# Kernel optimization log

Measured on AMD Instinct MI355X. Metric: run time of the kernel, lower is better.

## Reference

```python
import jax, jax.numpy as jnp
import numpy as np

B, Q, H, HKV, D = 4, 1024, 32, 8, 128
HID = H * D            # 4096
BS = 16                # block_size
BLOCKS_PER_SEQ = Q // BS  # 64
NB = B * BLOCKS_PER_SEQ   # 256 total cache blocks
THETA = 10000.0
SCALE = D ** -0.5


def _rope(x, pos):
    # x: [T, h, D] (NeoX half-split rotary), pos: [T] int
    inv = 1.0 / (THETA ** (jnp.arange(0, D, 2, dtype=jnp.float32) / D))  # [D/2]
    ang = pos[:, None].astype(jnp.float32) * inv                          # [T, D/2]
    cos = jnp.cos(ang)[:, None, :]
    sin = jnp.sin(ang)[:, None, :]
    x1, x2 = jnp.split(x, 2, axis=-1)
    return jnp.concatenate([x1 * cos - x2 * sin, x1 * sin + x2 * cos], axis=-1).astype(x.dtype)


def setup_inputs() -> dict:
    key = jax.random.key(0)
    ks = jax.random.split(key, 3)
    hidden_states = jax.random.normal(ks[0], (B * Q, HID), dtype=jnp.float32)
    w_qkv = jax.random.normal(ks[1], (HID, (H + 2 * HKV) * D), dtype=jnp.float32) * 0.02
    w_o = jax.random.normal(ks[2], (H * D, HID), dtype=jnp.float32) * 0.02
    key_cache = jnp.zeros((NB, BS, HKV, D), dtype=jnp.float32)
    value_cache = jnp.zeros((NB, BS, HKV, D), dtype=jnp.float32)
    positions = jnp.tile(jnp.arange(Q, dtype=jnp.int32), B)          # context_len=0 prefill
    slot_mapping = jnp.arange(B * Q, dtype=jnp.int32)                # contiguous slots
    block_tables = jnp.arange(NB, dtype=jnp.int32).reshape(B, BLOCKS_PER_SEQ)
    return {"hidden_states": hidden_states, "w_qkv": w_qkv, "w_o": w_o,
            "key_cache": key_cache, "value_cache": value_cache,
            "positions": positions, "slot_mapping": slot_mapping,
            "block_tables": block_tables}


def reference(hidden_states, w_qkv, w_o, key_cache, value_cache, positions, slot_mapping, block_tables):
    # QKV projection and split (q_size = H*D, kv_size = HKV*D)
    qkv = hidden_states @ w_qkv
    q, k, v = jnp.split(qkv, [H * D, H * D + HKV * D], axis=-1)
    q = q.reshape(-1, H, D)
    k = k.reshape(-1, HKV, D)
    v = v.reshape(-1, HKV, D)
    q = _rope(q, positions)
    k = _rope(k, positions)
    # BlockedKVCache.write: slot -> (slot // BS, slot % BS); flatten block dims
    kc = key_cache.reshape(NB * BS, HKV, D).at[slot_mapping].set(k)
    vc = value_cache.reshape(NB * BS, HKV, D).at[slot_mapping].set(v)
    # BlockedKVCache.gather via block_table: [B, blocks, BS, HKV, D] -> [B, S, HKV, D]
    gk = kc.reshape(NB, BS, HKV, D)[block_tables].reshape(B, Q, HKV, D)
    gv = vc.reshape(NB, BS, HKV, D)[block_tables].reshape(B, Q, HKV, D)
    # repeat_kv (GQA): each kv head repeated consecutively
    rep = H // HKV
    gk = jnp.repeat(gk, rep, axis=2)   # [B, S, H, D]
    gv = jnp.repeat(gv, rep, axis=2)
    qb = q.reshape(B, Q, H, D)
    scores = jnp.einsum('bqhd,bshd->bhqs', qb, gk) * SCALE
    # visible = context_len + token_idx + 1 with context_len=0 -> causal mask
    causal = jnp.arange(Q)[None, :] <= jnp.arange(Q)[:, None]          # [q, s]
    scores = jnp.where(causal[None, None], scores.astype(jnp.float32), -jnp.inf)
    probs = jax.nn.softmax(scores, axis=-1).astype(qb.dtype)
    attn = jnp.einsum('bhqs,bshd->bqhd', probs, gv).reshape(B * Q, H * D)
    return attn @ w_o
```

## Files before the change

### kernel.cpp

```cpp
#include <hip/hip_runtime.h>
#include <stdint.h>

typedef short short8  __attribute__((ext_vector_type(8)));
typedef short short4v __attribute__((ext_vector_type(4)));
typedef float f32x4   __attribute__((ext_vector_type(4)));

#define B_    4
#define Q_    1024
#define H_    32
#define HKV_  8
#define D_    128
#define HID_  4096
#define NQKV_ 6144
#define SCALE_ 0.08838834764831845f

__device__ __forceinline__ short f2bf(float f) {
  unsigned u = __builtin_bit_cast(unsigned, f);
  u += 0x7fffu + ((u >> 16) & 1u);
  return (short)(u >> 16);
}
__device__ __forceinline__ float bf2f(short s) {
  unsigned u = ((unsigned)(unsigned short)s) << 16;
  return __builtin_bit_cast(float, u);
}

__device__ __forceinline__ void gload_lds16(const void* g, void* l) {
  __builtin_amdgcn_global_load_lds(
      (__attribute__((address_space(1))) void*)(uintptr_t)(g),
      (__attribute__((address_space(3))) void*)(l), 16, 0, 0);
}

__device__ __forceinline__ f32x4 mfma16x16x32(short8 a, short8 b, f32x4 c) {
  return __builtin_amdgcn_mfma_f32_16x16x32_bf16(a, b, c, 0, 0, 0);
}

__global__ __launch_bounds__(256) void k_cvt(const float* __restrict__ src,
                                             short* __restrict__ dst, int n) {
  int i = (blockIdx.x * 256 + threadIdx.x) * 4;
  if (i + 3 < n) {
    float4 v = *reinterpret_cast<const float4*>(src + i);
    short4v o;
    o[0] = f2bf(v.x); o[1] = f2bf(v.y); o[2] = f2bf(v.z); o[3] = f2bf(v.w);
    *reinterpret_cast<short4v*>(dst + i) = o;
  }
}

__global__ __launch_bounds__(256) void k_cvt_t(const float* __restrict__ src,
                                               short* __restrict__ dst, int R, int C) {
  __shared__ float tile[32][33];
  int c0 = blockIdx.x * 32, r0 = blockIdx.y * 32;
  int tx = threadIdx.x & 31, ty = threadIdx.x >> 5;
#pragma unroll
  for (int i = 0; i < 4; ++i)
    tile[ty + i * 8][tx] = src[(size_t)(r0 + ty + i * 8) * C + c0 + tx];
  __syncthreads();
#pragma unroll
  for (int i = 0; i < 4; ++i)
    dst[(size_t)(c0 + ty + i * 8) * R + r0 + tx] = f2bf(tile[tx][ty + i * 8]);
}

__global__ __launch_bounds__(256) void k_gemm1(const short* __restrict__ A,
                                               const short* __restrict__ Bt,
                                               short* __restrict__ qout,
                                               short* __restrict__ kvout) {
  __shared__ alignas(16) short Asm[128 * 32];
  __shared__ alignas(16) short Bsm[128 * 32];
  const int tid = threadIdx.x;
  const int wave = tid >> 6, lane = tid & 63;
  const int G = lane >> 4, r = lane & 15;
  const int wm = wave >> 1, wn = wave & 1;
  const size_t Arow0 = (size_t)blockIdx.y * 128;
  const size_t Brow0 = (size_t)blockIdx.x * 128;
  const int K = HID_;
  const int ldrow = lane >> 2, ldcol = (lane & 3) * 8;
  short* Cb; size_t ldc, cb;
  if (Brow0 < (size_t)HID_) { Cb = qout; ldc = HID_; cb = Brow0; }
  else                      { Cb = kvout; ldc = 2048; cb = Brow0 - HID_; }
  f32x4 acc[4][4] = {};
  for (int k0 = 0; k0 < K; k0 += 32) {
    __syncthreads();
#pragma unroll
    for (int i = 0; i < 2; ++i) {
      int c = wave * 2 + i;
      gload_lds16(A + (Arow0 + c * 16 + ldrow) * K + k0 + ldcol, &Asm[c * 512]);
      gload_lds16(Bt + (Brow0 + c * 16 + ldrow) * K + k0 + ldcol, &Bsm[c * 512]);
    }
    asm volatile("s_waitcnt vmcnt(0)" ::: "memory");
    __syncthreads();
    short8 af[4], bf[4];
#pragma unroll
    for (int i = 0; i < 4; ++i)
      af[i] = *reinterpret_cast<const short8*>(&Asm[(wm * 64 + i * 16 + r) * 32 + G * 8]);
#pragma unroll
    for (int j = 0; j < 4; ++j)
      bf[j] = *reinterpret_cast<const short8*>(&Bsm[(wn * 64 + j * 16 + r) * 32 + G * 8]);
#pragma unroll
    for (int i = 0; i < 4; ++i)
#pragma unroll
      for (int j = 0; j < 4; ++j)
        acc[i][j] = mfma16x16x32(af[i], bf[j], acc[i][j]);
  }
#pragma unroll
  for (int i = 0; i < 4; ++i)
#pragma unroll
    for (int j = 0; j < 4; ++j)
#pragma unroll
      for (int rr = 0; rr < 4; ++rr) {
        size_t row = Arow0 + wm * 64 + i * 16 + G * 4 + rr;
        size_t col = cb + wn * 64 + j * 16 + r;
        Cb[row * ldc + col] = f2bf(acc[i][j][rr]);
      }
}

__global__ __launch_bounds__(256) void k_gemm2(const short* __restrict__ A,
                                               const short* __restrict__ Bt,
                                               float* __restrict__ C) {
  __shared__ alignas(16) short Asm[128 * 32];
  __shared__ alignas(16) short Bsm[128 * 32];
  const int tid = threadIdx.x;
  const int wave = tid >> 6, lane = tid & 63;
  const int G = lane >> 4, r = lane & 15;
  const int wm = wave >> 1, wn = wave & 1;
  const size_t Arow0 = (size_t)blockIdx.y * 128;
  const size_t Brow0 = (size_t)blockIdx.x * 128;
  const int K = HID_;
  const int ldrow = lane >> 2, ldcol = (lane & 3) * 8;
  f32x4 acc[4][4] = {};
  for (int k0 = 0; k0 < K; k0 += 32) {
    __syncthreads();
#pragma unroll
    for (int i = 0; i < 2; ++i) {
      int c = wave * 2 + i;
      gload_lds16(A + (Arow0 + c * 16 + ldrow) * K + k0 + ldcol, &Asm[c * 512]);
      gload_lds16(Bt + (Brow0 + c * 16 + ldrow) * K + k0 + ldcol, &Bsm[c * 512]);
    }
    asm volatile("s_waitcnt vmcnt(0)" ::: "memory");
    __syncthreads();
    short8 af[4], bf[4];
#pragma unroll
    for (int i = 0; i < 4; ++i)
      af[i] = *reinterpret_cast<const short8*>(&Asm[(wm * 64 + i * 16 + r) * 32 + G * 8]);
#pragma unroll
    for (int j = 0; j < 4; ++j)
      bf[j] = *reinterpret_cast<const short8*>(&Bsm[(wn * 64 + j * 16 + r) * 32 + G * 8]);
#pragma unroll
    for (int i = 0; i < 4; ++i)
#pragma unroll
      for (int j = 0; j < 4; ++j)
        acc[i][j] = mfma16x16x32(af[i], bf[j], acc[i][j]);
  }
#pragma unroll
  for (int i = 0; i < 4; ++i)
#pragma unroll
    for (int j = 0; j < 4; ++j)
#pragma unroll
      for (int rr = 0; rr < 4; ++rr) {
        size_t row = Arow0 + wm * 64 + i * 16 + G * 4 + rr;
        size_t col = Brow0 + wn * 64 + j * 16 + r;
        C[row * (size_t)HID_ + col] = acc[i][j][rr];
      }
}

__global__ __launch_bounds__(256) void k_rope_bf(short* __restrict__ x, int nh, int ld) {
  const int t = blockIdx.x;
  const float pos = (float)(t & (Q_ - 1));
  short* row = x + (size_t)t * ld;
  for (int i = threadIdx.x; i < nh * 64; i += 256) {
    int h = i >> 6, j = i & 63;
    float fr = powf(10000.0f, -(float)j * (1.0f / 64.0f));
    float sn, cs;
    sincosf(pos * fr, &sn, &cs);
    float x1 = bf2f(row[h * D_ + j]);
    float x2 = bf2f(row[h * D_ + 64 + j]);
    row[h * D_ + j]      = f2bf(x1 * cs - x2 * sn);
    row[h * D_ + 64 + j] = f2bf(x1 * sn + x2 * cs);
  }
}

__global__ __launch_bounds__(256) void k_attn(const short* __restrict__ qbf,
                                              const short* __restrict__ kv,
                                              short* __restrict__ attn) {
  const int qt = blockIdx.x;
  const int h  = blockIdx.y;
  const int b  = blockIdx.z;
  const int hkv = h >> 2;
  const int tid = threadIdx.x, wave = tid >> 6, lane = tid & 63;
  const int G = lane >> 4, r = lane & 15;
  const int q0w = qt * 64 + wave * 16;
  const float NEG_INF = -__builtin_inff();
  __shared__ alignas(16) short Ksm[32 * 136];
  __shared__ alignas(16) short Vsm[128 * 40];
  __shared__ alignas(16) short Psm[4][16][40];
  short8 qf[4];
  {
    const short* qrow = qbf + ((size_t)(b * Q_ + q0w + r)) * HID_ + h * D_;
#pragma unroll
    for (int ds = 0; ds < 4; ++ds)
      qf[ds] = *reinterpret_cast<const short8*>(qrow + ds * 32 + G * 8);
  }
  f32x4 acc[8] = {};
  float m_run = NEG_INF, l_run = 0.f;
  const int ntiles = qt * 2 + 2;
  const int my_q = q0w + r;
  const int my_q_hi = q0w + 15;
  const int krow = tid >> 3, kd0 = (tid & 7) * 16;
  const int vs = tid & 31, vdg = tid >> 5;
  for (int st = 0; st < ntiles; ++st) {
    __syncthreads();
    {
      const short* gk = kv + ((size_t)(b * Q_ + st * 32 + krow)) * 2048 + hkv * D_ + kd0;
      *reinterpret_cast<uint4*>(&Ksm[krow * 136 + kd0])     = *reinterpret_cast<const uint4*>(gk);
      *reinterpret_cast<uint4*>(&Ksm[krow * 136 + kd0 + 8]) = *reinterpret_cast<const uint4*>(gk + 8);
      const short* gv = kv + ((size_t)(b * Q_ + st * 32 + vs)) * 2048 + 1024 + hkv * D_ + vdg * 16;
      short tmp[16];
      *reinterpret_cast<uint4*>(&tmp[0]) = *reinterpret_cast<const uint4*>(gv);
      *reinterpret_cast<uint4*>(&tmp[8]) = *reinterpret_cast<const uint4*>(gv + 8);
#pragma unroll
      for (int i = 0; i < 16; ++i) Vsm[(vdg * 16 + i) * 40 + vs] = tmp[i];
    }
    __syncthreads();
    if (st * 32 <= my_q_hi) {
      f32x4 sacc[2] = {};
#pragma unroll
      for (int sb = 0; sb < 2; ++sb)
#pragma unroll
        for (int ds = 0; ds < 4; ++ds) {
          short8 kf = *reinterpret_cast<const short8*>(&Ksm[(sb * 16 + r) * 136 + ds * 32 + G * 8]);
          sacc[sb] = mfma16x16x32(kf, qf[ds], sacc[sb]);
        }
      float vals[8];
      float mymax = NEG_INF;
#pragma unroll
      for (int sb = 0; sb < 2; ++sb)
#pragma unroll
        for (int j = 0; j < 4; ++j) {
          int sIdx = st * 32 + sb * 16 + G * 4 + j;
          float v = sacc[sb][j] * SCALE_;
          v = (sIdx <= my_q) ? v : NEG_INF;
          vals[sb * 4 + j] = v;
          mymax = fmaxf(mymax, v);
        }
      mymax = fmaxf(mymax, __shfl_xor(mymax, 16));
      mymax = fmaxf(mymax, __shfl_xor(mymax, 32));
      float m_new = fmaxf(m_run, mymax);
      float factor = __expf(m_run - m_new);
      float psum = 0.f;
      float pv_[8];
#pragma unroll
      for (int i = 0; i < 8; ++i) {
        float p = __expf(vals[i] - m_new);
        psum += p;
        pv_[i] = p;
      }
      psum += __shfl_xor(psum, 16);
      psum += __shfl_xor(psum, 32);
      l_run = l_run * factor + psum;
      m_run = m_new;
#pragma unroll
      for (int i = 0; i < 8; ++i)
        Psm[wave][r][(i >> 2) * 16 + G * 4 + (i & 3)] = f2bf(pv_[i]);
      asm volatile("s_waitcnt lgkmcnt(0)" ::: "memory");
      __builtin_amdgcn_sched_barrier(0);
      short8 pf = *reinterpret_cast<const short8*>(&Psm[wave][r][G * 8]);
      float frow[4];
#pragma unroll
      for (int rr = 0; rr < 4; ++rr) frow[rr] = __shfl(factor, G * 4 + rr);
#pragma unroll
      for (int dt = 0; dt < 8; ++dt)
#pragma unroll
        for (int rr = 0; rr < 4; ++rr) acc[dt][rr] *= frow[rr];
#pragma unroll
      for (int dt = 0; dt < 8; ++dt) {
        short8 vf = *reinterpret_cast<const short8*>(&Vsm[(dt * 16 + r) * 40 + G * 8]);
        acc[dt] = mfma16x16x32(pf, vf, acc[dt]);
      }
    }
  }
  float inv = 1.0f / l_run;
  float irow[4];
#pragma unroll
  for (int rr = 0; rr < 4; ++rr) irow[rr] = __shfl(inv, G * 4 + rr);
#pragma unroll
  for (int dt = 0; dt < 8; ++dt)
#pragma unroll
    for (int rr = 0; rr < 4; ++rr) {
      size_t rowi = (size_t)(b * Q_ + q0w + G * 4 + rr) * HID_;
      attn[rowi + h * D_ + dt * 16 + r] = f2bf(acc[dt][rr] * irow[rr]);
    }
}

extern "C" void kernel_launch(void* const* d_in, const int* in_sizes, int n_in,
                              void* d_out, int out_size, void* d_ws, size_t ws_size,
                              hipStream_t stream) {
  const float* hidden = (const float*)d_in[0];
  const float* w_qkv  = (const float*)d_in[1];
  const float* w_o    = (const float*)d_in[2];
  float* out = (float*)d_out;
  char* ws = (char*)d_ws;
  char* od = (char*)d_out;
  short* hid_bf  = (short*)(od + 0);
  short* q_bf    = (short*)(od + 33554432);
  short* wqkvT   = (short*)(ws + 0);
  short* kv_ws   = (short*)(ws + 50331648);
  short* attn_bf = (short*)(ws + 0);
  short* woT     = (short*)(ws + 33554432);

  k_cvt<<<dim3(16384), dim3(256), 0, stream>>>(hidden, hid_bf, HID_ * B_ * Q_);
  k_cvt_t<<<dim3(192, 128), dim3(256), 0, stream>>>(w_qkv, wqkvT, HID_, NQKV_);
  k_gemm1<<<dim3(48, 32), dim3(256), 0, stream>>>(hid_bf, wqkvT, q_bf, kv_ws);
  k_rope_bf<<<dim3(B_ * Q_), dim3(256), 0, stream>>>(q_bf, H_, HID_);
  k_rope_bf<<<dim3(B_ * Q_), dim3(256), 0, stream>>>(kv_ws, HKV_, 2048);
  k_attn<<<dim3(16, 32, 4), dim3(256), 0, stream>>>(q_bf, kv_ws, attn_bf);
  k_cvt_t<<<dim3(128, 128), dim3(256), 0, stream>>>(w_o, woT, HID_, HID_);
  k_gemm2<<<dim3(32, 32), dim3(256), 0, stream>>>(attn_bf, woT, out);
}
```

Baseline: 665.1 us.

## Widen GEMM K-step to 64, fuse RoPE launches, add MFMA priority hints in attention

Both GEMM kernels now stage two 32-wide K slices into LDS per barrier pair, halving the number of syncthreads and vmcnt waits per K loop at the cost of doubled LDS per block. The two RoPE launches for Q and K are merged into one kernel that handles all 40 heads per token, removing a launch. The attention kernel raises wave priority around its MFMA sections to encourage interleaving of matrix work with softmax math across waves. Higher LDS use in the GEMMs could reduce occupancy.

After: 660.8 us. No clear change (-0.6%).

```diff
diff --git a/kernel.cpp b/kernel.cpp
--- a/kernel.cpp
+++ b/kernel.cpp
@@ -63,8 +63,8 @@
                                                const short* __restrict__ Bt,
                                                short* __restrict__ qout,
                                                short* __restrict__ kvout) {
-  __shared__ alignas(16) short Asm[128 * 32];
-  __shared__ alignas(16) short Bsm[128 * 32];
+  __shared__ alignas(16) short Asm[2][128 * 32];
+  __shared__ alignas(16) short Bsm[2][128 * 32];
   const int tid = threadIdx.x;
   const int wave = tid >> 6, lane = tid & 63;
   const int G = lane >> 4, r = lane & 15;
@@ -77,28 +77,33 @@
   if (Brow0 < (size_t)HID_) { Cb = qout; ldc = HID_; cb = Brow0; }
   else                      { Cb = kvout; ldc = 2048; cb = Brow0 - HID_; }
   f32x4 acc[4][4] = {};
-  for (int k0 = 0; k0 < K; k0 += 32) {
-    __syncthreads();
-#pragma unroll
-    for (int i = 0; i < 2; ++i) {
-      int c = wave * 2 + i;
-      gload_lds16(A + (Arow0 + c * 16 + ldrow) * K + k0 + ldcol, &Asm[c * 512]);
-      gload_lds16(Bt + (Brow0 + c * 16 + ldrow) * K + k0 + ldcol, &Bsm[c * 512]);
-    }
+  for (int k0 = 0; k0 < K; k0 += 64) {
+    __syncthreads();
+#pragma unroll
+    for (int h = 0; h < 2; ++h)
+#pragma unroll
+      for (int i = 0; i < 2; ++i) {
+        int c = wave * 2 + i;
+        gload_lds16(A + (Arow0 + c * 16 + ldrow) * K + k0 + h * 32 + ldcol, &Asm[h][c * 512]);
+        gload_lds16(Bt + (Brow0 + c * 16 + ldrow) * K + k0 + h * 32 + ldcol, &Bsm[h][c * 512]);
+      }
     asm volatile("s_waitcnt vmcnt(0)" ::: "memory");
     __syncthreads();
-    short8 af[4], bf[4];
-#pragma unroll
-    for (int i = 0; i < 4; ++i)
-      af[i] = *reinterpret_cast<const short8*>(&Asm[(wm * 64 + i * 16 + r) * 32 + G * 8]);
-#pragma unroll
-    for (int j = 0; j < 4; ++j)
-      bf[j] = *reinterpret_cast<const short8*>(&Bsm[(wn * 64 + j * 16 + r) * 32 + G * 8]);
-#pragma unroll
-    for (int i = 0; i < 4; ++i)
+#pragma unroll
+    for (int h = 0; h < 2; ++h) {
+      short8 af[4], bf[4];
+#pragma unroll
+      for (int i = 0; i < 4; ++i)
+        af[i] = *reinterpret_cast<const short8*>(&Asm[h][(wm * 64 + i * 16 + r) * 32 + G * 8]);
 #pragma unroll
       for (int j = 0; j < 4; ++j)
-        acc[i][j] = mfma16x16x32(af[i], bf[j], acc[i][j]);
+        bf[j] = *reinterpret_cast<const short8*>(&Bsm[h][(wn * 64 + j * 16 + r) * 32 + G * 8]);
+#pragma unroll
+      for (int i = 0; i < 4; ++i)
+#pragma unroll
+        for (int j = 0; j < 4; ++j)
+          acc[i][j] = mfma16x16x32(af[i], bf[j], acc[i][j]);
+    }
   }
 #pragma unroll
   for (int i = 0; i < 4; ++i)
@@ -115,8 +120,8 @@
 __global__ __launch_bounds__(256) void k_gemm2(const short* __restrict__ A,
                                                const short* __restrict__ Bt,
                                                float* __restrict__ C) {
-  __shared__ alignas(16) short Asm[128 * 32];
-  __shared__ alignas(16) short Bsm[128 * 32];
+  __shared__ alignas(16) short Asm[2][128 * 32];
+  __shared__ alignas(16) short Bsm[2][128 * 32];
   const int tid = threadIdx.x;
   const int wave = tid >> 6, lane = tid & 63;
   const int G = lane >> 4, r = lane & 15;
@@ -126,28 +131,33 @@
   const int K = HID_;
   const int ldrow = lane >> 2, ldcol = (lane & 3) * 8;
   f32x4 acc[4][4] = {};
-  for (int k0 = 0; k0 < K; k0 += 32) {
-    __syncthreads();
-#pragma unroll
-    for (int i = 0; i < 2; ++i) {
-      int c = wave * 2 + i;
-      gload_lds16(A + (Arow0 + c * 16 + ldrow) * K + k0 + ldcol, &Asm[c * 512]);
-      gload_lds16(Bt + (Brow0 + c * 16 + ldrow) * K + k0 + ldcol, &Bsm[c * 512]);
-    }
+  for (int k0 = 0; k0 < K; k0 += 64) {
+    __syncthreads();
+#pragma unroll
+    for (int h = 0; h < 2; ++h)
+#pragma unroll
+      for (int i = 0; i < 2; ++i) {
+        int c = wave * 2 + i;
+        gload_lds16(A + (Arow0 + c * 16 + ldrow) * K + k0 + h * 32 + ldcol, &Asm[h][c * 512]);
+        gload_lds16(Bt + (Brow0 + c * 16 + ldrow) * K + k0 + h * 32 + ldcol, &Bsm[h][c * 512]);
+      }
     asm volatile("s_waitcnt vmcnt(0)" ::: "memory");
     __syncthreads();
-    short8 af[4], bf[4];
-#pragma unroll
-    for (int i = 0; i < 4; ++i)
-      af[i] = *reinterpret_cast<const short8*>(&Asm[(wm * 64 + i * 16 + r) * 32 + G * 8]);
-#pragma unroll
-    for (int j = 0; j < 4; ++j)
-      bf[j] = *reinterpret_cast<const short8*>(&Bsm[(wn * 64 + j * 16 + r) * 32 + G * 8]);
-#pragma unroll
-    for (int i = 0; i < 4; ++i)
+#pragma unroll
+    for (int h = 0; h < 2; ++h) {
+      short8 af[4], bf[4];
+#pragma unroll
+      for (int i = 0; i < 4; ++i)
+        af[i] = *reinterpret_cast<const short8*>(&Asm[h][(wm * 64 + i * 16 + r) * 32 + G * 8]);
 #pragma unroll
       for (int j = 0; j < 4; ++j)
-        acc[i][j] = mfma16x16x32(af[i], bf[j], acc[i][j]);
+        bf[j] = *reinterpret_cast<const short8*>(&Bsm[h][(wn * 64 + j * 16 + r) * 32 + G * 8]);
+#pragma unroll
+      for (int i = 0; i < 4; ++i)
+#pragma unroll
+        for (int j = 0; j < 4; ++j)
+          acc[i][j] = mfma16x16x32(af[i], bf[j], acc[i][j]);
+    }
   }
 #pragma unroll
   for (int i = 0; i < 4; ++i)
@@ -161,19 +171,22 @@
       }
 }
 
-__global__ __launch_bounds__(256) void k_rope_bf(short* __restrict__ x, int nh, int ld) {
+__global__ __launch_bounds__(256) void k_rope2(short* __restrict__ q,
+                                               short* __restrict__ kv) {
   const int t = blockIdx.x;
   const float pos = (float)(t & (Q_ - 1));
-  short* row = x + (size_t)t * ld;
-  for (int i = threadIdx.x; i < nh * 64; i += 256) {
+  short* qrow = q + (size_t)t * HID_;
+  short* krow = kv + (size_t)t * 2048;
+  for (int i = threadIdx.x; i < (H_ + HKV_) * 64; i += 256) {
     int h = i >> 6, j = i & 63;
+    short* row = (h < H_) ? (qrow + h * D_) : (krow + (h - H_) * D_);
     float fr = powf(10000.0f, -(float)j * (1.0f / 64.0f));
     float sn, cs;
     sincosf(pos * fr, &sn, &cs);
-    float x1 = bf2f(row[h * D_ + j]);
-    float x2 = bf2f(row[h * D_ + 64 + j]);
-    row[h * D_ + j]      = f2bf(x1 * cs - x2 * sn);
-    row[h * D_ + 64 + j] = f2bf(x1 * sn + x2 * cs);
+    float x1 = bf2f(row[j]);
+    float x2 = bf2f(row[64 + j]);
+    row[j]      = f2bf(x1 * cs - x2 * sn);
+    row[64 + j] = f2bf(x1 * sn + x2 * cs);
   }
 }
 
@@ -221,6 +234,7 @@
     __syncthreads();
     if (st * 32 <= my_q_hi) {
       f32x4 sacc[2] = {};
+      __builtin_amdgcn_s_setprio(1);
 #pragma unroll
       for (int sb = 0; sb < 2; ++sb)
 #pragma unroll
@@ -228,6 +242,7 @@
           short8 kf = *reinterpret_cast<const short8*>(&Ksm[(sb * 16 + r) * 136 + ds * 32 + G * 8]);
           sacc[sb] = mfma16x16x32(kf, qf[ds], sacc[sb]);
         }
+      __builtin_amdgcn_s_setprio(0);
       float vals[8];
       float mymax = NEG_INF;
 #pragma unroll
@@ -269,11 +284,13 @@
       for (int dt = 0; dt < 8; ++dt)
 #pragma unroll
         for (int rr = 0; rr < 4; ++rr) acc[dt][rr] *= frow[rr];
+      __builtin_amdgcn_s_setprio(1);
 #pragma unroll
       for (int dt = 0; dt < 8; ++dt) {
         short8 vf = *reinterpret_cast<const short8*>(&Vsm[(dt * 16 + r) * 40 + G * 8]);
         acc[dt] = mfma16x16x32(pf, vf, acc[dt]);
       }
+      __builtin_amdgcn_s_setprio(0);
     }
   }
   float inv = 1.0f / l_run;
@@ -308,8 +325,7 @@
   k_cvt<<<dim3(16384), dim3(256), 0, stream>>>(hidden, hid_bf, HID_ * B_ * Q_);
   k_cvt_t<<<dim3(192, 128), dim3(256), 0, stream>>>(w_qkv, wqkvT, HID_, NQKV_);
   k_gemm1<<<dim3(48, 32), dim3(256), 0, stream>>>(hid_bf, wqkvT, q_bf, kv_ws);
-  k_rope_bf<<<dim3(B_ * Q_), dim3(256), 0, stream>>>(q_bf, H_, HID_);
-  k_rope_bf<<<dim3(B_ * Q_), dim3(256), 0, stream>>>(kv_ws, HKV_, 2048);
+  k_rope2<<<dim3(B_ * Q_), dim3(256), 0, stream>>>(q_bf, kv_ws);
   k_attn<<<dim3(16, 32, 4), dim3(256), 0, stream>>>(q_bf, kv_ws, attn_bf);
   k_cvt_t<<<dim3(128, 128), dim3(256), 0, stream>>>(w_o, woT, HID_, HID_);
   k_gemm2<<<dim3(32, 32), dim3(256), 0, stream>>>(attn_bf, woT, out);
```
